# Optimization experiments

Hardware: AMD Instinct MI355X
Metric: run time of the kernel (lower is better)

## Reference

```python
import jax, jax.numpy as jnp
import numpy as np

POOL = 7          # cf.pool_size
SR = 2            # roi_align sampling_ratio
LEVELS = [0, 1, 2, 3]
C = 192           # cf.end_filts
HC = 2            # cf.head_classes
RF = 1
N_ROIS = 1000
B = 4


def roi_align_2d(fmap, boxes, batch_inds, pool_size=POOL, sr=SR):
    """Bilinear RoIAlign. fmap [B,C,H,W]; boxes [N,4] = (y1,x1,y2,x2) in fmap pixel coords."""
    _, _, H, W = fmap.shape
    y1, x1, y2, x2 = boxes[:, 0], boxes[:, 1], boxes[:, 2], boxes[:, 3]
    bin_h = jnp.maximum(y2 - y1, 1.0) / pool_size
    bin_w = jnp.maximum(x2 - x1, 1.0) / pool_size
    # sampling offsets within the roi, [pool*sr]
    grid = (jnp.arange(pool_size, dtype=jnp.float32)[:, None]
            + (jnp.arange(sr, dtype=jnp.float32)[None, :] + 0.5) / sr).reshape(-1)
    ys = y1[:, None] + grid[None, :] * bin_h[:, None]   # [N, P*S]
    xs = x1[:, None] + grid[None, :] * bin_w[:, None]   # [N, P*S]
    y = jnp.broadcast_to(ys[:, :, None], (ys.shape[0], ys.shape[1], xs.shape[1]))  # [N,PS,PS]
    x = jnp.broadcast_to(xs[:, None, :], y.shape)
    valid = (y >= -1.0) & (y <= H) & (x >= -1.0) & (x <= W)
    y = jnp.clip(y, 0.0, H - 1)
    x = jnp.clip(x, 0.0, W - 1)
    y0 = jnp.floor(y).astype(jnp.int32)
    x0 = jnp.floor(x).astype(jnp.int32)
    y1i = jnp.minimum(y0 + 1, H - 1)
    x1i = jnp.minimum(x0 + 1, W - 1)
    ly = y - y0
    lx = x - x0
    b = batch_inds[:, None, None]
    f00 = fmap[b, :, y0, x0]    # [N,PS,PS,C]
    f01 = fmap[b, :, y0, x1i]
    f10 = fmap[b, :, y1i, x0]
    f11 = fmap[b, :, y1i, x1i]
    w00 = ((1 - ly) * (1 - lx))[..., None]
    w01 = ((1 - ly) * lx)[..., None]
    w10 = (ly * (1 - lx))[..., None]
    w11 = (ly * lx)[..., None]
    val = (f00 * w00 + f01 * w01 + f10 * w10 + f11 * w11) * valid[..., None]
    n = val.shape[0]
    val = val.reshape(n, pool_size, sr, pool_size, sr, -1).mean(axis=(2, 4))  # [N,P,P,C]
    return jnp.transpose(val, (0, 3, 1, 2))  # [N,C,P,P]


def pyramid_roi_align(fmaps, rois, pool_size=POOL, levels=LEVELS):
    boxes = jax.lax.stop_gradient(rois[:, :4])  # level_boxes.detach() in original
    batch_ix = rois[:, 4].astype(jnp.int32)
    h = boxes[:, 2] - boxes[:, 0]
    w = boxes[:, 3] - boxes[:, 1]
    roi_level = jnp.clip(jnp.round(4.0 + jnp.log2(jnp.sqrt(h * w))),
                         levels[0], levels[-1]).astype(jnp.int32)
    pooled = jnp.zeros((boxes.shape[0], fmaps[0].shape[1], pool_size, pool_size), fmaps[0].dtype)
    for li, lvl in enumerate(levels):
        H, W = fmaps[li].shape[2], fmaps[li].shape[3]
        scale = jnp.asarray([H, W, H, W], jnp.float32)
        p = roi_align_2d(fmaps[li], boxes * scale, batch_ix, pool_size)
        pooled = jnp.where((roi_level == lvl)[:, None, None, None], p, pooled)
    return pooled


def setup_inputs() -> dict:
    key = jax.random.key(0)
    ks = jax.random.split(key, 20)
    fmap0 = jax.random.normal(ks[0], (B, C, 128, 128), jnp.float32)
    fmap1 = jax.random.normal(ks[1], (B, C, 64, 64), jnp.float32)
    fmap2 = jax.random.normal(ks[2], (B, C, 32, 32), jnp.float32)
    fmap3 = jax.random.normal(ks[3], (B, C, 16, 16), jnp.float32)
    # valid normalized rois: (y1,x1,y2,x2,batch_ix)
    cy = jax.random.uniform(ks[4], (N_ROIS,), minval=0.15, maxval=0.85)
    cx = jax.random.uniform(ks[5], (N_ROIS,), minval=0.15, maxval=0.85)
    hh = jax.random.uniform(ks[6], (N_ROIS,), minval=0.02, maxval=0.15)
    hw = jax.random.uniform(ks[7], (N_ROIS,), minval=0.02, maxval=0.15)
    bix = jax.random.randint(ks[8], (N_ROIS,), 0, B).astype(jnp.float32)
    rois = jnp.stack([jnp.clip(cy - hh, 0, 1), jnp.clip(cx - hw, 0, 1),
                      jnp.clip(cy + hh, 0, 1), jnp.clip(cx + hw, 0, 1), bix], axis=1)
    d = C * 4  # 768
    s1 = 1.0 / np.sqrt(C * POOL * POOL)
    s2 = 1.0 / np.sqrt(d)
    params = dict(
        w1=jax.random.normal(ks[9], (d, C, POOL, POOL), jnp.float32) * s1,
        b1=jnp.zeros((d,), jnp.float32),
        w2=jax.random.normal(ks[10], (d, d), jnp.float32) * s2,
        b2=jnp.zeros((d,), jnp.float32),
        w_bbox=jax.random.normal(ks[11], (HC * 4, d), jnp.float32) * s2,
        b_bbox=jnp.zeros((HC * 4,), jnp.float32),
        w_cls=jax.random.normal(ks[12], (HC, d), jnp.float32) * s2,
        b_cls=jnp.zeros((HC,), jnp.float32),
        w_reg=jax.random.normal(ks[13], (HC * RF, d), jnp.float32) * s2,
        b_reg=jnp.zeros((HC * RF,), jnp.float32),
        w_unc=jax.random.normal(ks[14], (HC, d), jnp.float32) * s2,
        b_unc=jnp.zeros((HC,), jnp.float32),
    )
    return dict(fmap0=fmap0, fmap1=fmap1, fmap2=fmap2, fmap3=fmap3, rois=rois, **params)


def reference(fmap0, fmap1, fmap2, fmap3, rois, w1, b1, w2, b2,
              w_bbox, b_bbox, w_cls, b_cls, w_reg, b_reg, w_unc, b_unc):
    x = pyramid_roi_align([fmap0, fmap1, fmap2, fmap3], rois)      # [N,C,7,7]
    x = jax.nn.relu(jnp.einsum('ncij,ocij->no', x, w1) + b1)       # conv1 ks=7 -> 1x1
    x = jax.nn.relu(x @ w2.T + b2)                                 # conv2 1x1
    n = x.shape[0]
    mrcnn_bbox = (x @ w_bbox.T + b_bbox).reshape(n, -1, 4)         # [N,HC,2*dim]
    mrcnn_class_logits = x @ w_cls.T + b_cls                       # [N,HC]
    reg = (x @ w_reg.T + b_reg).reshape(n, -1, RF)
    unc = x @ w_unc.T + b_unc
    mrcnn_regress = jnp.concatenate([reg, unc[..., None]], axis=2)  # [N,HC,RF+1]
    return mrcnn_bbox, mrcnn_class_logits, mrcnn_regress
```

## Files before the change

### kernel.cpp

```cpp
#include <hip/hip_runtime.h>
#include <hip/hip_bf16.h>
#include <cstddef>
#include <cstdint>

typedef __attribute__((ext_vector_type(8))) short short8;
typedef __attribute__((ext_vector_type(16))) float float16;

#define C_CH 192
#define PK   9408
#define D1   768

__device__ __forceinline__ ushort f2bf(float v) {
    return __builtin_bit_cast(unsigned short, __float2bfloat16(v));
}

__global__ __launch_bounds__(256) void cvt_bf16_2(
    const float* __restrict__ in1, ushort* __restrict__ out1, int n4_1,
    const float* __restrict__ in2, ushort* __restrict__ out2, int n4_2)
{
    int i = blockIdx.x * 256 + threadIdx.x;
    const float* in; ushort* out;
    if (i < n4_1) { in = in1; out = out1; }
    else          { i -= n4_1; if (i >= n4_2) return; in = in2; out = out2; }
    float4 v = ((const float4*)in)[i];
    ushort4 o;
    o.x = f2bf(v.x); o.y = f2bf(v.y); o.z = f2bf(v.z); o.w = f2bf(v.w);
    ((ushort4*)out)[i] = o;
}

__global__ __launch_bounds__(256) void cvt_bf16(const float* __restrict__ in,
                                                ushort* __restrict__ out, int n4)
{
    int i = blockIdx.x * 256 + threadIdx.x;
    if (i >= n4) return;
    float4 v = ((const float4*)in)[i];
    ushort4 o;
    o.x = f2bf(v.x); o.y = f2bf(v.y); o.z = f2bf(v.z); o.w = f2bf(v.w);
    ((ushort4*)out)[i] = o;
}

__global__ __launch_bounds__(256) void fused_pre(
    const float* __restrict__ f0, const float* __restrict__ f1,
    const float* __restrict__ f2, const float* __restrict__ f3,
    ushort* __restrict__ o0, ushort* __restrict__ o1,
    ushort* __restrict__ o2, ushort* __restrict__ o3,
    const float* __restrict__ w1src, ushort* __restrict__ w1dst, int n41,
    const float* __restrict__ w2src, ushort* __restrict__ w2dst, int n42,
    int nTrans)
{
    __shared__ unsigned int sm[96][33];

    int bx = blockIdx.x;
    if (bx >= nTrans) {
        int i = (bx - nTrans) * 256 + threadIdx.x;
        const float* in; ushort* out;
        if (i < n41) { in = w1src; out = w1dst; }
        else         { i -= n41; if (i >= n42) return; in = w2src; out = w2dst; }
        float4 v = ((const float4*)in)[i];
        ushort4 o;
        o.x = f2bf(v.x); o.y = f2bf(v.y); o.z = f2bf(v.z); o.w = f2bf(v.w);
        ((ushort4*)out)[i] = o;
        return;
    }

    int b = bx / 680;
    int t = bx - b * 680;
    const float* in; ushort* out; int HW, hw0;
    if      (t < 512) { in = f0; out = o0; HW = 16384; hw0 = t * 32; }
    else if (t < 640) { in = f1; out = o1; HW = 4096;  hw0 = (t - 512) * 32; }
    else if (t < 672) { in = f2; out = o2; HW = 1024;  hw0 = (t - 640) * 32; }
    else              { in = f3; out = o3; HW = 256;   hw0 = (t - 672) * 32; }

    int tx = threadIdx.x & 31;
    int ty = threadIdx.x >> 5;

    const float* ip = in + (size_t)b * C_CH * HW + hw0;
    #pragma unroll
    for (int it = 0; it < 12; ++it) {
        int cp = it * 8 + ty;
        float v0 = ip[(size_t)(2 * cp)     * HW + tx];
        float v1 = ip[(size_t)(2 * cp + 1) * HW + tx];
        sm[cp][tx] = (unsigned int)f2bf(v0) | ((unsigned int)f2bf(v1) << 16);
    }
    __syncthreads();

    unsigned int* op = (unsigned int*)(out + ((size_t)b * HW + hw0) * C_CH);
    #pragma unroll
    for (int it = 0; it < 12; ++it) {
        int idx = it * 256 + (int)threadIdx.x;
        int r = idx / 96;
        int p = idx - r * 96;
        op[idx] = sm[p][r];
    }
}

__device__ __forceinline__ void issue16(
    const char* sbase, const int (*offB)[4], const float (*wt)[4],
    int s4, int c4, unsigned int* u, float* w)
{
    #pragma unroll
    for (int k = 0; k < 16; ++k) {
        int s  = s4 + (k >> 2);
        int tp = k & 3;
        u[k] = *(const unsigned int*)(sbase + (offB[s][tp] + c4));
        w[k] = wt[s][tp];
    }
}

__device__ __forceinline__ void comp16(
    const unsigned int* u, const float* w, float& a0, float& a1)
{
    #pragma unroll
    for (int k = 0; k < 16; ++k) {
        float lo = __builtin_bit_cast(float, u[k] << 16);
        float hi = __builtin_bit_cast(float, u[k] & 0xffff0000u);
        a0 = fmaf(lo, w[k], a0);
        a1 = fmaf(hi, w[k], a1);
    }
}

__global__ __launch_bounds__(192) void roi_gather(
    const ushort* __restrict__ n0p, const ushort* __restrict__ n1p,
    const ushort* __restrict__ n2p, const ushort* __restrict__ n3p,
    const float* __restrict__ rois, ushort* __restrict__ pooled)
{
    __shared__ int    s_offB[196][4];
    __shared__ float  s_w[196][4];
    __shared__ ushort s_out[96 * 49];

    const int n    = blockIdx.x >> 1;
    const int half = blockIdx.x & 1;
    const int tid  = threadIdx.x;

    float by1 = rois[n*5+0], bx1 = rois[n*5+1];
    float by2 = rois[n*5+2], bx2 = rois[n*5+3];
    int   b   = (int)rois[n*5+4];

    float hh = by2 - by1, ww = bx2 - bx1;
    int lvl = (int)rintf(4.0f + log2f(sqrtf(hh * ww)));
    lvl = min(max(lvl, 0), 3);

    const ushort* fm; int H;
    if      (lvl == 0) { fm = n0p; H = 128; }
    else if (lvl == 1) { fm = n1p; H = 64;  }
    else if (lvl == 2) { fm = n2p; H = 32;  }
    else               { fm = n3p; H = 16;  }
    float Hf = (float)H;

    float y1p = by1 * Hf, x1p = bx1 * Hf;
    float y2p = by2 * Hf, x2p = bx2 * Hf;
    float bin_h = fmaxf(y2p - y1p, 1.0f) * (1.0f / 7.0f);
    float bin_w = fmaxf(x2p - x1p, 1.0f) * (1.0f / 7.0f);

    uintptr_t bp = (uintptr_t)(fm + (size_t)b * H * H * C_CH);
    unsigned int blo = __builtin_amdgcn_readfirstlane((unsigned int)bp);
    unsigned int bhi = __builtin_amdgcn_readfirstlane((unsigned int)(bp >> 32));
    const char* sbase = (const char*)((((uintptr_t)bhi) << 32) | blo);

    for (int s = tid; s < 196; s += 192) {
        int sx = s & 1, sy = (s >> 1) & 1, ij = s >> 2;
        int i = ij / 7, j = ij - i * 7;

        float gy = (float)i + 0.25f + 0.5f * (float)sy;
        float y  = y1p + gy * bin_h;
        bool  vy = (y >= -1.0f) && (y <= Hf);
        float yc = fminf(fmaxf(y, 0.0f), Hf - 1.0f);
        int   y0 = (int)floorf(yc);
        float ly = yc - (float)y0;
        int   y1i = min(y0 + 1, H - 1);

        float gx = (float)j + 0.25f + 0.5f * (float)sx;
        float x  = x1p + gx * bin_w;
        bool  vx = (x >= -1.0f) && (x <= Hf);
        float xc = fminf(fmaxf(x, 0.0f), Hf - 1.0f);
        int   x0 = (int)floorf(xc);
        float lx = xc - (float)x0;
        int   x1i = min(x0 + 1, H - 1);

        float vm = (vy && vx) ? 0.25f : 0.0f;
        s_offB[s][0] = (y0  * H + x0 ) * (C_CH * 2);
        s_offB[s][1] = (y0  * H + x1i) * (C_CH * 2);
        s_offB[s][2] = (y1i * H + x0 ) * (C_CH * 2);
        s_offB[s][3] = (y1i * H + x1i) * (C_CH * 2);
        s_w[s][0] = (1.0f - ly) * (1.0f - lx) * vm;
        s_w[s][1] = (1.0f - ly) * lx * vm;
        s_w[s][2] = ly * (1.0f - lx) * vm;
        s_w[s][3] = ly * lx * vm;
    }
    __syncthreads();

    const int grp = tid / 48;
    const int ci  = tid - grp * 48;
    const int cl  = ci * 2;
    const int c4  = (half * 96 + cl) * 2;
    const int bin_lo = grp * 13;
    const int bin_hi = min(bin_lo + 13, 49);

    unsigned int ua[16], ub[16];
    float        wa[16], wb[16];

    issue16(sbase, s_offB, s_w, bin_lo * 4, c4, ua, wa);
    int bin = bin_lo;
    while (true) {
        if (bin + 1 < bin_hi) issue16(sbase, s_offB, s_w, (bin + 1) * 4, c4, ub, wb);
        {
            float a0 = 0.0f, a1 = 0.0f;
            comp16(ua, wa, a0, a1);
            s_out[(cl + 0) * 49 + bin] = f2bf(a0);
            s_out[(cl + 1) * 49 + bin] = f2bf(a1);
        }
        if (++bin >= bin_hi) break;
        if (bin + 1 < bin_hi) issue16(sbase, s_offB, s_w, (bin + 1) * 4, c4, ua, wa);
        {
            float a0 = 0.0f, a1 = 0.0f;
            comp16(ub, wb, a0, a1);
            s_out[(cl + 0) * 49 + bin] = f2bf(a0);
            s_out[(cl + 1) * 49 + bin] = f2bf(a1);
        }
        if (++bin >= bin_hi) break;
    }
    __syncthreads();

    unsigned int* po = (unsigned int*)(pooled + (size_t)n * PK + half * 4704);
    const unsigned int* so = (const unsigned int*)s_out;
    for (int idx = tid; idx < 2352; idx += 192) po[idx] = so[idx];
}

__global__ __launch_bounds__(256) void roi_align_nchw(
    const float* __restrict__ f0, const float* __restrict__ f1,
    const float* __restrict__ f2, const float* __restrict__ f3,
    const float* __restrict__ rois, ushort* __restrict__ pooled, int n_rois)
{
    int idx = blockIdx.x * 256 + threadIdx.x;
    if (idx >= n_rois * PK) return;
    int n  = idx / PK;
    int r  = idx - n * PK;
    int c  = r / 49;
    int ij = r - c * 49;
    int i  = ij / 7;
    int j  = ij - i * 7;

    float by1 = rois[n*5+0], bx1 = rois[n*5+1];
    float by2 = rois[n*5+2], bx2 = rois[n*5+3];
    int   b   = (int)rois[n*5+4];

    float hh = by2 - by1, ww = bx2 - bx1;
    int lvl = (int)rintf(4.0f + log2f(sqrtf(hh * ww)));
    lvl = min(max(lvl, 0), 3);

    const float* fmap; int H;
    if      (lvl == 0) { fmap = f0; H = 128; }
    else if (lvl == 1) { fmap = f1; H = 64;  }
    else if (lvl == 2) { fmap = f2; H = 32;  }
    else               { fmap = f3; H = 16;  }
    float Hf = (float)H;

    float y1p = by1 * Hf, x1p = bx1 * Hf;
    float bin_h = fmaxf(by2 * Hf - y1p, 1.0f) * (1.0f / 7.0f);
    float bin_w = fmaxf(bx2 * Hf - x1p, 1.0f) * (1.0f / 7.0f);

    const float* base = fmap + ((size_t)b * C_CH + c) * (size_t)(H * H);

    float acc = 0.0f;
    #pragma unroll
    for (int sy = 0; sy < 2; ++sy) {
        float y  = y1p + ((float)i + 0.25f + 0.5f * (float)sy) * bin_h;
        bool  vy = (y >= -1.0f) && (y <= Hf);
        float yc = fminf(fmaxf(y, 0.0f), Hf - 1.0f);
        int   y0 = (int)floorf(yc);
        float ly = yc - (float)y0;
        int   y1i = min(y0 + 1, H - 1);
        #pragma unroll
        for (int sx = 0; sx < 2; ++sx) {
            float x  = x1p + ((float)j + 0.25f + 0.5f * (float)sx) * bin_w;
            bool  vx = (x >= -1.0f) && (x <= Hf);
            float xc = fminf(fmaxf(x, 0.0f), Hf - 1.0f);
            int   x0 = (int)floorf(xc);
            float lx = xc - (float)x0;
            int   x1i = min(x0 + 1, H - 1);
            if (vy && vx) {
                float v = base[y0 * H + x0 ] * (1.0f - ly) * (1.0f - lx)
                        + base[y0 * H + x1i] * (1.0f - ly) * lx
                        + base[y1i * H + x0 ] * ly * (1.0f - lx)
                        + base[y1i * H + x1i] * ly * lx;
                acc += v;
            }
        }
    }
    pooled[idx] = f2bf(acc * 0.25f);
}

template<int MODE>
__global__ __launch_bounds__(256) void mfma_gemm(
    const ushort* __restrict__ A, const ushort* __restrict__ W,
    const float* __restrict__ bias, void* __restrict__ outp,
    int M, int N, int K, int nkPer, int nkTotal)
{
    __shared__ char ldsA[2][8192];
    __shared__ char ldsB[2][8192];

    const int t    = threadIdx.x;
    const int lane = t & 63;
    const int wave = t >> 6;
    const int wm = wave >> 1, wn = wave & 1;

    const int m0 = blockIdx.y * 64;
    const int n0 = blockIdx.x * 64;
    const int kb = (MODE == 2) ? blockIdx.z * nkPer : 0;
    const int nk = (MODE == 2) ? min(nkPer, nkTotal - kb) : nkPer;

    const int ks   = t & 3;
    const int mrow = t >> 2;
    const int g    = mrow >> 5;
    const int rw   = mrow & 31;
    const int lof0 = ks*2048 + g*1024 + ((     rw) ^ (ks<<2))*16;
    const int lof1 = ks*2048 + g*1024 + ((32 + rw) ^ (ks<<2))*16;

    const int arow = min(m0 + mrow, M-1);
    const int brow = n0 + mrow;
    const ushort* ap = A + (size_t)arow * K + (size_t)kb * 64 + ks*16;
    const ushort* bp = W + (size_t)brow * K + (size_t)kb * 64 + ks*16;

    float4 ra0, ra1, rb0, rb1;
    float4 qa0, qa1, qb0, qb1;

    ra0 = ((const float4*)ap)[0]; ra1 = ((const float4*)ap)[1];
    rb0 = ((const float4*)bp)[0]; rb1 = ((const float4*)bp)[1];
    *(float4*)&ldsA[0][lof0] = ra0; *(float4*)&ldsA[0][lof1] = ra1;
    *(float4*)&ldsB[0][lof0] = rb0; *(float4*)&ldsB[0][lof1] = rb1;
    {
        int k1 = min(1, nk - 1);
        const ushort* ap1 = ap + (size_t)k1 * 64;
        const ushort* bp1 = bp + (size_t)k1 * 64;
        ra0 = ((const float4*)ap1)[0]; ra1 = ((const float4*)ap1)[1];
        rb0 = ((const float4*)bp1)[0]; rb1 = ((const float4*)bp1)[1];
    }
    __syncthreads();

    float16 acc = {};

    for (int kt = 0; kt < nk; ++kt) {
        {
            int k2 = min(kt + 2, nk - 1);
            const ushort* ap2 = ap + (size_t)k2 * 64;
            const ushort* bp2 = bp + (size_t)k2 * 64;
            qa0 = ((const float4*)ap2)[0]; qa1 = ((const float4*)ap2)[1];
            qb0 = ((const float4*)bp2)[0]; qb1 = ((const float4*)bp2)[1];
        }
        if (kt + 1 < nk) {
            char* dA = ldsA[(kt+1)&1]; char* dB = ldsB[(kt+1)&1];
            *(float4*)&dA[lof0] = ra0; *(float4*)&dA[lof1] = ra1;
            *(float4*)&dB[lof0] = rb0; *(float4*)&dB[lof1] = rb1;
        }
        const char* sA = ldsA[kt&1]; const char* sB = ldsB[kt&1];
        #pragma unroll
        for (int s = 0; s < 4; ++s) {
            int ro = s*2048 + (lane ^ (s<<2))*16;
            short8 af = *(const short8*)&sA[wm*1024 + ro];
            short8 bf = *(const short8*)&sB[wn*1024 + ro];
            acc = __builtin_amdgcn_mfma_f32_32x32x16_bf16(af, bf, acc, 0, 0, 0);
        }
        __syncthreads();
        ra0 = qa0; ra1 = qa1; rb0 = qb0; rb1 = qb1;
    }

    const int col   = lane & 31;
    const int rbase = 4 * (lane >> 5);
    const int nG    = n0 + wn*32 + col;

    if (MODE == 2) {
        float* O = (float*)outp + (size_t)blockIdx.z * M * N;
        #pragma unroll
        for (int r = 0; r < 16; ++r) {
            int row = (r & 3) + 8*(r >> 2) + rbase;
            int mG  = m0 + wm*32 + row;
            if (mG < M) O[(size_t)mG * N + nG] = acc[r];
        }
    } else if (MODE == 1) {
        const float bv = bias[nG];
        ushort* O = (ushort*)outp;
        #pragma unroll
        for (int r = 0; r < 16; ++r) {
            int row = (r & 3) + 8*(r >> 2) + rbase;
            int mG  = m0 + wm*32 + row;
            if (mG < M) O[(size_t)mG * N + nG] = f2bf(fmaxf(acc[r] + bv, 0.0f));
        }
    } else {
        const float bv = bias[nG];
        float* O = (float*)outp;
        #pragma unroll
        for (int r = 0; r < 16; ++r) {
            int row = (r & 3) + 8*(r >> 2) + rbase;
            int mG  = m0 + wm*32 + row;
            if (mG < M) O[(size_t)mG * N + nG] = fmaxf(acc[r] + bv, 0.0f);
        }
    }
}

__global__ __launch_bounds__(256) void reduce_relu_bf16(
    const float* __restrict__ P, const float* __restrict__ bias,
    ushort* __restrict__ Y, int MN, int N, int S)
{
    int idx = blockIdx.x * 256 + threadIdx.x;
    if (idx >= MN / 4) return;
    float4 s = ((const float4*)P)[idx];
    for (int k = 1; k < S; ++k) {
        float4 p = ((const float4*)(P + (size_t)k * MN))[idx];
        s.x += p.x; s.y += p.y; s.z += p.z; s.w += p.w;
    }
    int n4 = idx % (N / 4);
    float4 bv = ((const float4*)bias)[n4];
    ushort4 o;
    o.x = f2bf(fmaxf(s.x + bv.x, 0.0f));
    o.y = f2bf(fmaxf(s.y + bv.y, 0.0f));
    o.z = f2bf(fmaxf(s.z + bv.z, 0.0f));
    o.w = f2bf(fmaxf(s.w + bv.w, 0.0f));
    ((ushort4*)Y)[idx] = o;
}

__global__ __launch_bounds__(256) void reduce_heads(
    const float* __restrict__ P2, const float* __restrict__ b2, int S, int MN,
    const float* __restrict__ w_bbox, const float* __restrict__ b_bbox,
    const float* __restrict__ w_cls,  const float* __restrict__ b_cls,
    const float* __restrict__ w_reg,  const float* __restrict__ b_reg,
    const float* __restrict__ w_unc,  const float* __restrict__ b_unc,
    float* __restrict__ out, int n_rois)
{
    __shared__ float zrow[D1];
    const int m   = blockIdx.x;
    const int tid = threadIdx.x;

    const float* Pm = P2 + (size_t)m * D1;
    #pragma unroll
    for (int r = 0; r < 3; ++r) {
        int k = r * 256 + tid;
        float v = Pm[k];
        for (int s = 1; s < S; ++s) v += Pm[(size_t)s * MN + k];
        zrow[k] = fmaxf(v + b2[k], 0.0f);
    }
    __syncthreads();

    const int wave = tid >> 6;
    const int lane = tid & 63;
    for (int o = wave; o < 14; o += 4) {
        const float* w; float bb;
        if      (o < 8)  { w = w_bbox + o * D1;        bb = b_bbox[o]; }
        else if (o < 10) { w = w_cls  + (o - 8) * D1;  bb = b_cls[o - 8]; }
        else if (o < 12) { w = w_reg  + (o - 10) * D1; bb = b_reg[o - 10]; }
        else             { w = w_unc  + (o - 12) * D1; bb = b_unc[o - 12]; }
        float p = 0.0f;
        #pragma unroll
        for (int r = 0; r < 12; ++r) {
            int k = r * 64 + lane;
            p = fmaf(zrow[k], w[k], p);
        }
        #pragma unroll
        for (int d = 32; d >= 1; d >>= 1) p += __shfl_down(p, d, 64);
        if (lane == 0) {
            int off;
            int clsOff = n_rois * 8;
            int regOff = n_rois * 10;
            if      (o < 8)  off = m * 8 + o;
            else if (o < 10) off = clsOff + m * 2 + (o - 8);
            else if (o < 12) off = regOff + m * 4 + (o - 10) * 2;
            else             off = regOff + m * 4 + (o - 12) * 2 + 1;
            out[off] = p + bb;
        }
    }
}

__global__ __launch_bounds__(256) void heads_kernel(
    const float* __restrict__ Z,
    const float* __restrict__ w_bbox, const float* __restrict__ b_bbox,
    const float* __restrict__ w_cls,  const float* __restrict__ b_cls,
    const float* __restrict__ w_reg,  const float* __restrict__ b_reg,
    const float* __restrict__ w_unc,  const float* __restrict__ b_unc,
    float* __restrict__ out, int n_rois)
{
    int idx = blockIdx.x * 256 + threadIdx.x;
    if (idx >= n_rois * 14) return;
    int n = idx / 14;
    int o = idx - n * 14;

    const float* w; float bb;
    if      (o < 8)  { w = w_bbox + o * D1;        bb = b_bbox[o]; }
    else if (o < 10) { w = w_cls  + (o - 8) * D1;  bb = b_cls[o - 8]; }
    else if (o < 12) { w = w_reg  + (o - 10) * D1; bb = b_reg[o - 10]; }
    else             { w = w_unc  + (o - 12) * D1; bb = b_unc[o - 12]; }

    const float* z = Z + (size_t)n * D1;
    float s = bb;
    for (int k = 0; k < D1; k += 4) {
        float4 zv = *(const float4*)(z + k);
        float4 wv = *(const float4*)(w + k);
        s = fmaf(zv.x, wv.x, s);
        s = fmaf(zv.y, wv.y, s);
        s = fmaf(zv.z, wv.z, s);
        s = fmaf(zv.w, wv.w, s);
    }

    int off;
    int clsOff = n_rois * 8;
    int regOff = n_rois * 10;
    if      (o < 8)  off = n * 8 + o;
    else if (o < 10) off = clsOff + n * 2 + (o - 8);
    else if (o < 12) off = regOff + n * 4 + (o - 10) * 2;
    else             off = regOff + n * 4 + (o - 12) * 2 + 1;
    out[off] = s;
}

extern "C" void kernel_launch(void* const* d_in, const int* in_sizes, int n_in,
                              void* d_out, int out_size, void* d_ws, size_t ws_size,
                              hipStream_t stream)
{
    const float* f0   = (const float*)d_in[0];
    const float* f1   = (const float*)d_in[1];
    const float* f2   = (const float*)d_in[2];
    const float* f3   = (const float*)d_in[3];
    const float* rois = (const float*)d_in[4];
    const float* w1   = (const float*)d_in[5];
    const float* b1   = (const float*)d_in[6];
    const float* w2   = (const float*)d_in[7];
    const float* b2   = (const float*)d_in[8];
    const float* w_bbox = (const float*)d_in[9];
    const float* b_bbox = (const float*)d_in[10];
    const float* w_cls  = (const float*)d_in[11];
    const float* b_cls  = (const float*)d_in[12];
    const float* w_reg  = (const float*)d_in[13];
    const float* b_reg  = (const float*)d_in[14];
    const float* w_unc  = (const float*)d_in[15];
    const float* b_unc  = (const float*)d_in[16];
    float* out = (float*)d_out;

    const int n_rois = in_sizes[4] / 5;
    const int B      = in_sizes[0] / (C_CH * 128 * 128);

    const size_t nh0B = (size_t)B * 16384 * C_CH * 2;
    const size_t nh1B = (size_t)B * 4096  * C_CH * 2;
    const size_t nh2B = (size_t)B * 1024  * C_CH * 2;
    const size_t nh3B = (size_t)B * 256   * C_CH * 2;
    const size_t nhAll = nh0B + nh1B + nh2B + nh3B;
    const size_t poolB = (size_t)n_rois * PK * 2;
    const size_t w1Bb  = (size_t)D1 * PK * 2;
    const size_t w2Bb  = (size_t)D1 * D1 * 2;
    const size_t Yb    = (size_t)n_rois * D1 * 2;
    const size_t Zb    = (size_t)n_rois * D1 * 4;
    const size_t smallB = w2Bb + Yb + Zb;

    const int SPLIT1 = 5;
    const int SPLIT2 = 2;

    const size_t P1b   = (size_t)SPLIT1 * n_rois * D1 * 4;
    const size_t needX2 = nhAll + poolB + w1Bb + w2Bb + Yb;
    const size_t needX  = nhAll + poolB + smallB;

    char* ws = (char*)d_ws;

    int n41 = D1*PK/4, n42 = D1*D1/4;

    if (ws_size >= needX2) {
        ushort* nh0 = (ushort*)ws;
        ushort* nh1 = nh0 + nh0B/2;
        ushort* nh2 = nh1 + nh1B/2;
        ushort* nh3 = nh2 + nh2B/2;
        ushort* pooledB = (ushort*)(ws + nhAll);
        ushort* w1B = (ushort*)(ws + nhAll + poolB);
        ushort* w2B = (ushort*)(ws + nhAll + poolB + w1Bb);
        ushort* Y   = (ushort*)(ws + nhAll + poolB + w1Bb + w2Bb);
        float*  P   = (float*)ws;
        float*  P2  = (float*)(ws + P1b);

        int nTrans = 680 * B;
        int nCvt   = (n41 + n42 + 255) / 256;
        fused_pre<<<nTrans + nCvt, 256, 0, stream>>>(
            f0, f1, f2, f3, nh0, nh1, nh2, nh3,
            w1, w1B, n41, w2, w2B, n42, nTrans);

        roi_gather<<<2 * n_rois, 192, 0, stream>>>(nh0, nh1, nh2, nh3, rois, pooledB);

        {
            int nkTotal = PK / 64;
            int nkPer   = (nkTotal + SPLIT1 - 1) / SPLIT1;
            dim3 grid(D1/64, (n_rois + 63)/64, SPLIT1);
            mfma_gemm<2><<<grid, 256, 0, stream>>>(pooledB, w1B, nullptr, P,
                                                   n_rois, D1, PK, nkPer, nkTotal);
            int MN = n_rois * D1;
            reduce_relu_bf16<<<(MN/4 + 255)/256, 256, 0, stream>>>(P, b1, Y, MN, D1, SPLIT1);
        }
        {
            int nkTotal = D1 / 64;
            int nkPer   = nkTotal / SPLIT2;
            dim3 grid(D1/64, (n_rois + 63)/64, SPLIT2);
            mfma_gemm<2><<<grid, 256, 0, stream>>>(Y, w2B, nullptr, P2,
                                                   n_rois, D1, D1, nkPer, nkTotal);
            int MN = n_rois * D1;
            reduce_heads<<<n_rois, 256, 0, stream>>>(P2, b2, SPLIT2, MN,
                w_bbox, b_bbox, w_cls, b_cls, w_reg, b_reg, w_unc, b_unc, out, n_rois);
        }
    } else if (ws_size >= needX) {
        ushort* nh0 = (ushort*)ws;
        ushort* nh1 = nh0 + nh0B/2;
        ushort* nh2 = nh1 + nh1B/2;
        ushort* nh3 = nh2 + nh2B/2;
        ushort* w1B = (ushort*)ws;
        float*  P   = (float*)(ws + w1Bb);
        float*  P2  = (float*)ws;
        ushort* pooledB = (ushort*)(ws + nhAll);
        ushort* w2B = (ushort*)(ws + nhAll + poolB);
        ushort* Y   = w2B + w2Bb/2;

        int nTrans = 680 * B;
        fused_pre<<<nTrans, 256, 0, stream>>>(
            f0, f1, f2, f3, nh0, nh1, nh2, nh3,
            w1, (ushort*)nullptr, 0, w2, (ushort*)nullptr, 0, nTrans);
        roi_gather<<<2 * n_rois, 192, 0, stream>>>(nh0, nh1, nh2, nh3, rois, pooledB);
        cvt_bf16_2<<<(n41 + n42 + 255)/256, 256, 0, stream>>>(
            w1, w1B, n41, w2, w2B, n42);
        {
            int nkTotal = PK / 64;
            int nkPer   = (nkTotal + SPLIT1 - 1) / SPLIT1;
            dim3 grid(D1/64, (n_rois + 63)/64, SPLIT1);
            mfma_gemm<2><<<grid, 256, 0, stream>>>(pooledB, w1B, nullptr, P,
                                                   n_rois, D1, PK, nkPer, nkTotal);
            int MN = n_rois * D1;
            reduce_relu_bf16<<<(MN/4 + 255)/256, 256, 0, stream>>>(P, b1, Y, MN, D1, SPLIT1);
        }
        {
            int nkTotal = D1 / 64;
            int nkPer   = nkTotal / SPLIT2;
            dim3 grid(D1/64, (n_rois + 63)/64, SPLIT2);
            mfma_gemm<2><<<grid, 256, 0, stream>>>(Y, w2B, nullptr, P2,
                                                   n_rois, D1, D1, nkPer, nkTotal);
            int MN = n_rois * D1;
            reduce_heads<<<n_rois, 256, 0, stream>>>(P2, b2, SPLIT2, MN,
                w_bbox, b_bbox, w_cls, b_cls, w_reg, b_reg, w_unc, b_unc, out, n_rois);
        }
    } else {
        ushort* pooledB = (ushort*)ws;
        ushort* w1B = pooledB + poolB/2;
        ushort* w2B = w1B + w1Bb/2;
        ushort* Y   = w2B + w2Bb/2;
        float*  Z   = (float*)((char*)Y + Yb);

        cvt_bf16<<<((D1*PK/4) + 255)/256, 256, 0, stream>>>(w1, w1B, D1*PK/4);
        cvt_bf16<<<((D1*D1/4) + 255)/256, 256, 0, stream>>>(w2, w2B, D1*D1/4);
        {
            int total = n_rois * PK;
            roi_align_nchw<<<(total + 255)/256, 256, 0, stream>>>(
                f0, f1, f2, f3, rois, pooledB, n_rois);
        }
        {
            dim3 grid(D1/64, (n_rois + 63)/64);
            mfma_gemm<1><<<grid, 256, 0, stream>>>(pooledB, w1B, b1, Y,
                                                   n_rois, D1, PK, PK/64, PK/64);
        }
        {
            dim3 grid(D1/64, (n_rois + 63)/64);
            mfma_gemm<0><<<grid, 256, 0, stream>>>(Y, w2B, b2, Z,
                                                   n_rois, D1, D1, D1/64, D1/64);
        }
        heads_kernel<<<(n_rois*14 + 255)/256, 256, 0, stream>>>(
            Z, w_bbox, b_bbox, w_cls, b_cls, w_reg, b_reg, w_unc, b_unc, out, n_rois);
    }
}
```

Measured before the change: 228.8 us.

## Stage ROI patches in LDS and add 128x128 split-K GEMM tile

The ROI gather kernel now loads the whole bounding patch of feature pixels for each ROI into shared memory when it fits in 256 pixels, then does the bilinear sampling from LDS instead of repeated global loads. The old register double-buffered issue/compute loop is replaced by a simple loop. Separately, a new 128x128-tile MFMA GEMM kernel with register prefetch is used for conv1 in the main workspace path, with split-K raised from 5 to 10. The larger split writes more fp32 partials that the reduction kernel must read, and the big LDS allocation in roi_gather may limit occupancy.

```diff
diff --git a/kernel.cpp b/kernel.cpp
--- a/kernel.cpp
+++ b/kernel.cpp
@@ -94,37 +94,13 @@
     }
 }
 
-__device__ __forceinline__ void issue16(
-    const char* sbase, const int (*offB)[4], const float (*wt)[4],
-    int s4, int c4, unsigned int* u, float* w)
-{
-    #pragma unroll
-    for (int k = 0; k < 16; ++k) {
-        int s  = s4 + (k >> 2);
-        int tp = k & 3;
-        u[k] = *(const unsigned int*)(sbase + (offB[s][tp] + c4));
-        w[k] = wt[s][tp];
-    }
-}
-
-__device__ __forceinline__ void comp16(
-    const unsigned int* u, const float* w, float& a0, float& a1)
-{
-    #pragma unroll
-    for (int k = 0; k < 16; ++k) {
-        float lo = __builtin_bit_cast(float, u[k] << 16);
-        float hi = __builtin_bit_cast(float, u[k] & 0xffff0000u);
-        a0 = fmaf(lo, w[k], a0);
-        a1 = fmaf(hi, w[k], a1);
-    }
-}
-
 __global__ __launch_bounds__(192) void roi_gather(
     const ushort* __restrict__ n0p, const ushort* __restrict__ n1p,
     const ushort* __restrict__ n2p, const ushort* __restrict__ n3p,
     const float* __restrict__ rois, ushort* __restrict__ pooled)
 {
-    __shared__ int    s_offB[196][4];
+    __shared__ float4 s_patch4[256 * 12];
+    __shared__ int    s_off[196][4];
     __shared__ float  s_w[196][4];
     __shared__ ushort s_out[96 * 49];
 
@@ -151,6 +127,19 @@
     float y2p = by2 * Hf, x2p = bx2 * Hf;
     float bin_h = fmaxf(y2p - y1p, 1.0f) * (1.0f / 7.0f);
     float bin_w = fmaxf(x2p - x1p, 1.0f) * (1.0f / 7.0f);
+
+    float yF = fminf(fmaxf(y1p + 0.25f * bin_h, 0.0f), Hf - 1.0f);
+    float yL = fminf(fmaxf(y1p + 6.75f * bin_h, 0.0f), Hf - 1.0f);
+    float xF = fminf(fmaxf(x1p + 0.25f * bin_w, 0.0f), Hf - 1.0f);
+    float xL = fminf(fmaxf(x1p + 6.75f * bin_w, 0.0f), Hf - 1.0f);
+    int ymin = (int)floorf(yF);
+    int ymax = min((int)floorf(yL) + 1, H - 1);
+    int xmin = (int)floorf(xF);
+    int xmax = min((int)floorf(xL) + 1, H - 1);
+    int nrows = ymax - ymin + 1;
+    int ncols = xmax - xmin + 1;
+    int np = nrows * ncols;
+    bool usePatch = (np <= 256);
 
     uintptr_t bp = (uintptr_t)(fm + (size_t)b * H * H * C_CH);
     unsigned int blo = __builtin_amdgcn_readfirstlane((unsigned int)bp);
@@ -178,46 +167,88 @@
         int   x1i = min(x0 + 1, H - 1);
 
         float vm = (vy && vx) ? 0.25f : 0.0f;
-        s_offB[s][0] = (y0  * H + x0 ) * (C_CH * 2);
-        s_offB[s][1] = (y0  * H + x1i) * (C_CH * 2);
-        s_offB[s][2] = (y1i * H + x0 ) * (C_CH * 2);
-        s_offB[s][3] = (y1i * H + x1i) * (C_CH * 2);
+        if (usePatch) {
+            int ry0 = y0 - ymin, ry1 = y1i - ymin;
+            int rx0 = x0 - xmin, rx1 = x1i - xmin;
+            s_off[s][0] = (ry0 * ncols + rx0) * 48;
+            s_off[s][1] = (ry0 * ncols + rx1) * 48;
+            s_off[s][2] = (ry1 * ncols + rx0) * 48;
+            s_off[s][3] = (ry1 * ncols + rx1) * 48;
+        } else {
+            s_off[s][0] = (y0  * H + x0 ) * (C_CH * 2);
+            s_off[s][1] = (y0  * H + x1i) * (C_CH * 2);
+            s_off[s][2] = (y1i * H + x0 ) * (C_CH * 2);
+            s_off[s][3] = (y1i * H + x1i) * (C_CH * 2);
+        }
         s_w[s][0] = (1.0f - ly) * (1.0f - lx) * vm;
         s_w[s][1] = (1.0f - ly) * lx * vm;
         s_w[s][2] = ly * (1.0f - lx) * vm;
         s_w[s][3] = ly * lx * vm;
     }
+
+    if (usePatch) {
+        int pq = tid / 12;
+        int pd = tid - pq * 12;
+        for (int p0 = 0; p0 < np; p0 += 16) {
+            int p = p0 + pq;
+            if (p < np) {
+                int py = p / ncols;
+                int px = p - py * ncols;
+                const char* src = sbase +
+                    ((size_t)((ymin + py) * H + (xmin + px)) * (C_CH * 2)
+                     + half * 192 + pd * 16);
+                s_patch4[p * 12 + pd] = *(const float4*)src;
+            }
+        }
+    }
     __syncthreads();
 
     const int grp = tid / 48;
     const int ci  = tid - grp * 48;
     const int cl  = ci * 2;
-    const int c4  = (half * 96 + cl) * 2;
     const int bin_lo = grp * 13;
     const int bin_hi = min(bin_lo + 13, 49);
 
-    unsigned int ua[16], ub[16];
-    float        wa[16], wb[16];
-
-    issue16(sbase, s_offB, s_w, bin_lo * 4, c4, ua, wa);
-    int bin = bin_lo;
-    while (true) {
-        if (bin + 1 < bin_hi) issue16(sbase, s_offB, s_w, (bin + 1) * 4, c4, ub, wb);
-        {
+    if (usePatch) {
+        const unsigned int* patch_dw = (const unsigned int*)s_patch4;
+        for (int bin = bin_lo; bin < bin_hi; ++bin) {
             float a0 = 0.0f, a1 = 0.0f;
-            comp16(ua, wa, a0, a1);
+            #pragma unroll
+            for (int sub = 0; sub < 4; ++sub) {
+                int s = bin * 4 + sub;
+                #pragma unroll
+                for (int tp = 0; tp < 4; ++tp) {
+                    unsigned int u = patch_dw[s_off[s][tp] + ci];
+                    float w = s_w[s][tp];
+                    float lo = __builtin_bit_cast(float, u << 16);
+                    float hi = __builtin_bit_cast(float, u & 0xffff0000u);
+                    a0 = fmaf(lo, w, a0);
+                    a1 = fmaf(hi, w, a1);
+                }
+            }
             s_out[(cl + 0) * 49 + bin] = f2bf(a0);
             s_out[(cl + 1) * 49 + bin] = f2bf(a1);
         }
-        if (++bin >= bin_hi) break;
-        if (bin + 1 < bin_hi) issue16(sbase, s_offB, s_w, (bin + 1) * 4, c4, ua, wa);
-        {
+    } else {
+        const int c4g = half * 192 + ci * 4;
+        for (int bin = bin_lo; bin < bin_hi; ++bin) {
             float a0 = 0.0f, a1 = 0.0f;
-            comp16(ub, wb, a0, a1);
+            #pragma unroll
+            for (int sub = 0; sub < 4; ++sub) {
+                int s = bin * 4 + sub;
+                #pragma unroll
+                for (int tp = 0; tp < 4; ++tp) {
+                    unsigned int u = *(const unsigned int*)(sbase + (s_off[s][tp] + c4g));
+                    float w = s_w[s][tp];
+                    float lo = __builtin_bit_cast(float, u << 16);
+                    float hi = __builtin_bit_cast(float, u & 0xffff0000u);
+                    a0 = fmaf(lo, w, a0);
+                    a1 = fmaf(hi, w, a1);
+                }
+            }
             s_out[(cl + 0) * 49 + bin] = f2bf(a0);
             s_out[(cl + 1) * 49 + bin] = f2bf(a1);
         }
-        if (++bin >= bin_hi) break;
     }
     __syncthreads();
 
@@ -397,6 +428,123 @@
     }
 }
 
+__global__ __launch_bounds__(256) void mfma_gemm128(
+    const ushort* __restrict__ A, const ushort* __restrict__ W,
+    void* __restrict__ outp, int M, int N, int K, int nkPer, int nkTotal)
+{
+    __shared__ char ldsA[2][16384];
+    __shared__ char ldsB[2][16384];
+
+    const int t    = threadIdx.x;
+    const int lane = t & 63;
+    const int wave = t >> 6;
+    const int wm = wave >> 1, wn = wave & 1;
+
+    const int m0 = blockIdx.y * 128;
+    const int n0 = blockIdx.x * 128;
+    const int kb = blockIdx.z * nkPer;
+    const int nk = min(nkPer, nkTotal - kb);
+
+    const int ks   = t & 3;
+    const int mrow = t >> 2;
+    const int g    = mrow >> 5;
+    const int rw   = mrow & 31;
+    const int swz  = ks << 2;
+    const int lof0 = ks*4096 + g*1024 + ((     rw) ^ swz)*16;
+    const int lof1 = ks*4096 + g*1024 + ((32 + rw) ^ swz)*16;
+
+    const int arow0 = min(m0 + mrow,      M-1);
+    const int arow1 = min(m0 + mrow + 64, M-1);
+    const int brow0 = n0 + mrow;
+    const int brow1 = n0 + mrow + 64;
+    const ushort* ap0 = A + (size_t)arow0 * K + (size_t)kb * 64 + ks*16;
+    const ushort* ap1 = A + (size_t)arow1 * K + (size_t)kb * 64 + ks*16;
+    const ushort* bp0 = W + (size_t)brow0 * K + (size_t)kb * 64 + ks*16;
+    const ushort* bp1 = W + (size_t)brow1 * K + (size_t)kb * 64 + ks*16;
+
+    float4 ra0, ra1, ra2, ra3, rb0, rb1, rb2, rb3;
+    float4 qa0, qa1, qa2, qa3, qb0, qb1, qb2, qb3;
+
+    ra0 = ((const float4*)ap0)[0]; ra1 = ((const float4*)ap0)[1];
+    ra2 = ((const float4*)ap1)[0]; ra3 = ((const float4*)ap1)[1];
+    rb0 = ((const float4*)bp0)[0]; rb1 = ((const float4*)bp0)[1];
+    rb2 = ((const float4*)bp1)[0]; rb3 = ((const float4*)bp1)[1];
+    *(float4*)&ldsA[0][lof0]      = ra0; *(float4*)&ldsA[0][lof1]      = ra1;
+    *(float4*)&ldsA[0][lof0+2048] = ra2; *(float4*)&ldsA[0][lof1+2048] = ra3;
+    *(float4*)&ldsB[0][lof0]      = rb0; *(float4*)&ldsB[0][lof1]      = rb1;
+    *(float4*)&ldsB[0][lof0+2048] = rb2; *(float4*)&ldsB[0][lof1+2048] = rb3;
+    {
+        int k1 = min(1, nk - 1);
+        const ushort* a0 = ap0 + (size_t)k1 * 64; const ushort* a1 = ap1 + (size_t)k1 * 64;
+        const ushort* b0 = bp0 + (size_t)k1 * 64; const ushort* b1 = bp1 + (size_t)k1 * 64;
+        ra0 = ((const float4*)a0)[0]; ra1 = ((const float4*)a0)[1];
+        ra2 = ((const float4*)a1)[0]; ra3 = ((const float4*)a1)[1];
+        rb0 = ((const float4*)b0)[0]; rb1 = ((const float4*)b0)[1];
+        rb2 = ((const float4*)b1)[0]; rb3 = ((const float4*)b1)[1];
+    }
+    __syncthreads();
+
+    float16 acc00 = {}, acc01 = {}, acc10 = {}, acc11 = {};
+
+    for (int kt = 0; kt < nk; ++kt) {
+        {
+            int k2 = min(kt + 2, nk - 1);
+            const ushort* a0 = ap0 + (size_t)k2 * 64; const ushort* a1 = ap1 + (size_t)k2 * 64;
+            const ushort* b0 = bp0 + (size_t)k2 * 64; const ushort* b1 = bp1 + (size_t)k2 * 64;
+            qa0 = ((const float4*)a0)[0]; qa1 = ((const float4*)a0)[1];
+            qa2 = ((const float4*)a1)[0]; qa3 = ((const float4*)a1)[1];
+            qb0 = ((const float4*)b0)[0]; qb1 = ((const float4*)b0)[1];
+            qb2 = ((const float4*)b1)[0]; qb3 = ((const float4*)b1)[1];
+        }
+        if (kt + 1 < nk) {
+            char* dA = ldsA[(kt+1)&1]; char* dB = ldsB[(kt+1)&1];
+            *(float4*)&dA[lof0]      = ra0; *(float4*)&dA[lof1]      = ra1;
+            *(float4*)&dA[lof0+2048] = ra2; *(float4*)&dA[lof1+2048] = ra3;
+            *(float4*)&dB[lof0]      = rb0; *(float4*)&dB[lof1]      = rb1;
+            *(float4*)&dB[lof0+2048] = rb2; *(float4*)&dB[lof1+2048] = rb3;
+        }
+        const char* sA = ldsA[kt&1]; const char* sB = ldsB[kt&1];
+        #pragma unroll
+        for (int s = 0; s < 4; ++s) {
+            int ro = s*4096 + (lane ^ (s<<2))*16;
+            short8 a0 = *(const short8*)&sA[wm*2048        + ro];
+            short8 a1 = *(const short8*)&sA[wm*2048 + 1024 + ro];
+            short8 b0 = *(const short8*)&sB[wn*2048        + ro];
+            short8 b1 = *(const short8*)&sB[wn*2048 + 1024 + ro];
+            acc00 = __builtin_amdgcn_mfma_f32_32x32x16_bf16(a0, b0, acc00, 0, 0, 0);
+            acc01 = __builtin_amdgcn_mfma_f32_32x32x16_bf16(a0, b1, acc01, 0, 0, 0);
+            acc10 = __builtin_amdgcn_mfma_f32_32x32x16_bf16(a1, b0, acc10, 0, 0, 0);
+            acc11 = __builtin_amdgcn_mfma_f32_32x32x16_bf16(a1, b1, acc11, 0, 0, 0);
+        }
+        __syncthreads();
+        ra0 = qa0; ra1 = qa1; ra2 = qa2; ra3 = qa3;
+        rb0 = qb0; rb1 = qb1; rb2 = qb2; rb3 = qb3;
+    }
+
+    const int col   = lane & 31;
+    const int rbase = 4 * (lane >> 5);
+    float* O = (float*)outp + (size_t)blockIdx.z * M * N;
+
+    const int mb0 = m0 + wm*64;
+    const int nb0 = n0 + wn*64;
+    #pragma unroll
+    for (int r = 0; r < 16; ++r) {
+        int row = (r & 3) + 8*(r >> 2) + rbase;
+        int mG0 = mb0 + row;
+        int mG1 = mb0 + 32 + row;
+        int nG0 = nb0 + col;
+        int nG1 = nb0 + 32 + col;
+        if (mG0 < M) {
+            O[(size_t)mG0 * N + nG0] = acc00[r];
+            O[(size_t)mG0 * N + nG1] = acc01[r];
+        }
+        if (mG1 < M) {
+            O[(size_t)mG1 * N + nG0] = acc10[r];
+            O[(size_t)mG1 * N + nG1] = acc11[r];
+        }
+    }
+}
+
 __global__ __launch_bounds__(256) void reduce_relu_bf16(
     const float* __restrict__ P, const float* __restrict__ bias,
     ushort* __restrict__ Y, int MN, int N, int S)
@@ -547,8 +695,9 @@
     const size_t Zb    = (size_t)n_rois * D1 * 4;
     const size_t smallB = w2Bb + Yb + Zb;
 
-    const int SPLIT1 = 5;
-    const int SPLIT2 = 2;
+    const int SPLIT1  = 10;
+    const int SPLIT1F = 5;
+    const int SPLIT2  = 2;
 
     const size_t P1b   = (size_t)SPLIT1 * n_rois * D1 * 4;
     const size_t needX2 = nhAll + poolB + w1Bb + w2Bb + Yb;
@@ -581,8 +730,8 @@
         {
             int nkTotal = PK / 64;
             int nkPer   = (nkTotal + SPLIT1 - 1) / SPLIT1;
-            dim3 grid(D1/64, (n_rois + 63)/64, SPLIT1);
-            mfma_gemm<2><<<grid, 256, 0, stream>>>(pooledB, w1B, nullptr, P,
+            dim3 grid(D1/128, (n_rois + 127)/128, SPLIT1);
+            mfma_gemm128<<<grid, 256, 0, stream>>>(pooledB, w1B, P,
                                                    n_rois, D1, PK, nkPer, nkTotal);
             int MN = n_rois * D1;
             reduce_relu_bf16<<<(MN/4 + 255)/256, 256, 0, stream>>>(P, b1, Y, MN, D1, SPLIT1);
@@ -618,12 +767,12 @@
             w1, w1B, n41, w2, w2B, n42);
         {
             int nkTotal = PK / 64;
-            int nkPer   = (nkTotal + SPLIT1 - 1) / SPLIT1;
-            dim3 grid(D1/64, (n_rois + 63)/64, SPLIT1);
+            int nkPer   = (nkTotal + SPLIT1F - 1) / SPLIT1F;
+            dim3 grid(D1/64, (n_rois + 63)/64, SPLIT1F);
             mfma_gemm<2><<<grid, 256, 0, stream>>>(pooledB, w1B, nullptr, P,
                                                    n_rois, D1, PK, nkPer, nkTotal);
             int MN = n_rois * D1;
-            reduce_relu_bf16<<<(MN/4 + 255)/256, 256, 0, stream>>>(P, b1, Y, MN, D1, SPLIT1);
+            reduce_relu_bf16<<<(MN/4 + 255)/256, 256, 0, stream>>>(P, b1, Y, MN, D1, SPLIT1F);
         }
         {
             int nkTotal = D1 / 64;
```

Measured after the change: 241.5 us. 5.6% more time.
